# Kernel optimization log

Measured on AMD Instinct MI355X. Metric: run time of the kernel, lower is better.

Reference implementation:

```python
import jax, jax.numpy as jnp
import numpy as np

B, T, D_MODEL = 2, 2048, 2048
N, H, R = 1024, 16, 512
DH = 128          # mem_head_dim (even, fully rotated: rope_dim == DH)
MLAT = 128        # mem_latent_dim
TOPK = 64
EPS = 1e-6
ROPE_BASE = 10000.0


def _rms_norm(x, w):
    var = jnp.mean(jnp.square(x), axis=-1, keepdims=True)
    return x * jax.lax.rsqrt(var + EPS) * w


def _rotate_half(x):
    x1, x2 = jnp.split(x, 2, axis=-1)
    return jnp.concatenate([-x2, x1], axis=-1)


def _apply_rope(x, positions):
    # x: [B, H, L, DH], positions: [L] -> cos/sin [1, 1, L, DH]
    inv_freq = 1.0 / (ROPE_BASE ** (jnp.arange(0, DH, 2, dtype=jnp.float32) / DH))
    freqs = positions.astype(jnp.float32)[:, None] * inv_freq  # [L, DH/2]
    emb = jnp.concatenate([freqs, freqs], axis=-1)             # [L, DH]
    cos = jnp.cos(emb)[None, None].astype(x.dtype)
    sin = jnp.sin(emb)[None, None].astype(x.dtype)
    return x * cos + _rotate_half(x) * sin


def setup_inputs() -> dict:
    key = jax.random.key(0)
    ks = jax.random.split(key, 16)
    s = 0.02
    return {
        "x": jax.random.normal(ks[0], (B, T, D_MODEL), jnp.float32),
        "snapshots": jax.random.normal(ks[1], (B, N, H, R), jnp.float32),
        "snap_positions": jnp.sort(jax.random.randint(ks[2], (N,), 0, T)),
        "token_offset": 0,
        "Wq_down": jax.random.normal(ks[3], (D_MODEL, MLAT), jnp.float32) * s,
        "Wq_up": jax.random.normal(ks[4], (MLAT, H * DH), jnp.float32) * s,
        "Wg_down": jax.random.normal(ks[5], (D_MODEL, MLAT), jnp.float32) * s,
        "Wg_up": jax.random.normal(ks[6], (MLAT, H * DH), jnp.float32) * s,
        "Wo_down": jax.random.normal(ks[7], (H * DH, MLAT), jnp.float32) * s,
        "Wo_up": jax.random.normal(ks[8], (MLAT, D_MODEL), jnp.float32) * s,
        "Wk_up": jax.random.normal(ks[9], (R, DH), jnp.float32) * s,
        "Wv_up": jax.random.normal(ks[10], (R, DH), jnp.float32) * s,
        "q_norm_w": jnp.ones((DH,), jnp.float32),
        "k_norm_w": jnp.ones((DH,), jnp.float32),
        "sink_logit": jnp.zeros((H,), jnp.float32),
    }


def reference(x, snapshots, snap_positions, token_offset,
              Wq_down, Wq_up, Wg_down, Wg_up, Wo_down, Wo_up,
              Wk_up, Wv_up, q_norm_w, k_norm_w, sink_logit):
    b, t, d = x.shape
    _, n, h, r = snapshots.shape
    dh = DH

    # Q path: down/up projection, per-head RMSNorm -> [B, H, T, DH]
    q = ((x @ Wq_down) @ Wq_up).reshape(b, t, h, dh)
    q = _rms_norm(q, q_norm_w).transpose(0, 2, 1, 3)

    # K/V from snapshot latents: [B, N, H, DH] -> [B, H, N, DH]
    k = _rms_norm(snapshots @ Wk_up, k_norm_w).transpose(0, 2, 1, 3)
    v = (snapshots @ Wv_up).transpose(0, 2, 1, 3)

    # dual RoPE: Q by absolute token position, K by snapshot end position
    t_abs = token_offset + jnp.arange(t)
    q = _apply_rope(q, t_abs)
    k = _apply_rope(k, snap_positions)

    scores = jnp.einsum('bhtd,bhnd->bhtn', q, k) / jnp.sqrt(jnp.asarray(dh, q.dtype))

    # causal mask: snapshot strictly before token
    valid = (snap_positions[None, :] < t_abs[:, None])[None, None]  # [1,1,T,N]
    neg_inf = jnp.asarray(-jnp.inf, scores.dtype)
    scores = jnp.where(valid, scores, neg_inf)

    # causal top-k: keep entries >= k-th largest per (b,h,t)
    k_sel = min(TOPK, n)
    if k_sel < n:
        top_vals, _ = jax.lax.top_k(scores, k_sel)
        kth = top_vals[..., -1:]
        scores = jnp.where(scores >= kth, scores, neg_inf)

    # attention sink: extra learned logit per head
    sink = jnp.broadcast_to(sink_logit.astype(jnp.float32)[None, :, None, None], (b, h, t, 1))
    aug = jnp.concatenate([scores.astype(jnp.float32), sink], axis=-1)
    weights = jax.nn.softmax(aug, axis=-1)[..., :n].astype(v.dtype)

    out = jnp.einsum('bhtn,bhnd->bhtd', weights, v)
    out = out.transpose(0, 2, 1, 3).reshape(b, t, h * dh)

    gate = jax.nn.sigmoid((x @ Wg_down) @ Wg_up)
    out = out * gate
    out = (out @ Wo_down) @ Wo_up
    return out
```

## Files before the change

kernel.cpp:

```cpp
#include <hip/hip_runtime.h>

typedef unsigned short u16;
typedef unsigned int u32;
typedef __attribute__((ext_vector_type(8))) short bf16x8;
typedef __attribute__((ext_vector_type(8))) _Float16 f16x8;
typedef __attribute__((ext_vector_type(4))) float f32x4;

__device__ __forceinline__ float b2f(u16 u) {
  union { u32 i; float f; } v; v.i = ((u32)u) << 16; return v.f;
}
__device__ __forceinline__ u16 f2b(float f) {
  u32 u = __builtin_bit_cast(u32, f);
  u32 r = u + 0x7FFFu + ((u >> 16) & 1u);
  return (u16)(r >> 16);
}
__device__ __forceinline__ u16 f2h(float f) {
  return __builtin_bit_cast(u16, (_Float16)f);
}
__device__ __forceinline__ float h2f(u16 u) {
  return (float)__builtin_bit_cast(_Float16, u);
}
__device__ __forceinline__ float wsum(float v) {
  #pragma unroll
  for (int o = 32; o; o >>= 1) v += __shfl_xor(v, o);
  return v;
}
__device__ __forceinline__ float wmax(float v) {
  #pragma unroll
  for (int o = 32; o; o >>= 1) v = fmaxf(v, __shfl_xor(v, o));
  return v;
}

__global__ void k_detect(const u32* x, int* flag) {
  int lane = threadIdx.x;
  u32 w = x[lane * 131 + 7];
  float v = b2f((u16)(w & 0xFFFF));
  float a = fabsf(v);
  bool sane = (a > 1e-3f) && (a < 100.0f);
  unsigned long long m = __ballot(sane);
  if (lane == 0) flag[0] = (__popcll(m) >= 32) ? 0 : 1;
}

struct WtArgs {
  const void* s[8];
  const void* vq; const void* vk; const void* vs;
};
__global__ __launch_bounds__(256)
void k_wtrans_all(WtArgs a, u16* wb, const int* flag) {
  __shared__ u16 Ts[64][66];
  int id = blockIdx.x, t = threadIdx.x, dt = flag[0];
  if (id == 416) {
    u16* dq = wb + 1703936; u16* dk = wb + 1704064; u16* ds = wb + 1704192;
    if (t < 128) dq[t] = dt ? f2b(((const float*)a.vq)[t]) : ((const u16*)a.vq)[t];
    else if (t < 256) dk[t-128] = dt ? f2b(((const float*)a.vk)[t-128]) : ((const u16*)a.vk)[t-128];
    if (t < 16) ds[t] = dt ? f2b(((const float*)a.vs)[t]) : ((const u16*)a.vs)[t];
    return;
  }
  const int cum[9] = {0,64,128,144,160,224,288,352,416};
  const int gsh[8] = {1,1,1,1,5,5,1,5};
  const int Ks[8]  = {2048,2048,512,512,128,128,2048,128};
  const int Ns[8]  = {128,128,128,128,2048,2048,128,2048};
  const unsigned dsts[8] = {0,262144,524288,589824,655360,917504,1179648,1441792};
  int seg = 0;
  #pragma unroll
  for (int i = 0; i < 7; ++i) seg += (id >= cum[i+1]);
  int rel = id - cum[seg];
  int bx = rel & ((1 << gsh[seg]) - 1), by = rel >> gsh[seg];
  int K = Ks[seg], N = Ns[seg];
  const void* src = a.s[seg];
  u16* dst = wb + dsts[seg];
  int col0 = bx * 64, k0 = by * 64;
  int lr = t >> 4, lc = (t & 15) * 4;
  if (dt) {
    #pragma unroll
    for (int p = 0; p < 4; ++p) {
      int kr = lr + p * 16;
      float4 v = *(const float4*)((const float*)src + (size_t)(k0 + kr) * N + col0 + lc);
      Ts[kr][lc+0] = f2b(v.x); Ts[kr][lc+1] = f2b(v.y);
      Ts[kr][lc+2] = f2b(v.z); Ts[kr][lc+3] = f2b(v.w);
    }
  } else {
    #pragma unroll
    for (int p = 0; p < 4; ++p) {
      int kr = lr + p * 16;
      uint2 v = *(const uint2*)((const u16*)src + (size_t)(k0 + kr) * N + col0 + lc);
      *(uint2*)&Ts[kr][lc] = v;
    }
  }
  __syncthreads();
  int col = t >> 2, ks = (t & 3) * 16;
  u16 tmp[16];
  #pragma unroll
  for (int i = 0; i < 16; ++i) tmp[i] = Ts[ks + i][col];
  u16* dp = dst + (size_t)(col0 + col) * K + k0 + ks;
  *(uint4*)dp = *(uint4*)&tmp[0];
  *(uint4*)(dp + 8) = *(uint4*)&tmp[8];
}

template<int JW>
__device__ __forceinline__ void skinny_body(const void* A, const u16* BT, u16* C0, u16* C1,
    int K, bool a32, int m0, int tid, u16 (*As)[40]) {
  int wave = tid >> 6, lane = tid & 63, quad = lane >> 4, l16 = lane & 15;
  f32x4 acc[JW];
  #pragma unroll
  for (int j = 0; j < JW; ++j) acc[j] = (f32x4){0.f,0.f,0.f,0.f};
  int row32 = tid >> 4, kp32 = (tid & 15) * 2;
  int row16 = tid >> 2, kp16 = (tid & 3) * 8;
  float2 pf32 = {};
  uint4 pf16 = {};
  if (a32) pf32 = *(const float2*)((const float*)A + (size_t)(m0+row32)*K + kp32);
  else if (tid < 64) pf16 = *(const uint4*)((const u16*)A + (size_t)(m0+row16)*K + kp16);
  uint4 bf[JW];
  #pragma unroll
  for (int j = 0; j < JW; ++j) {
    int col = wave*(JW*16) + j*16 + l16;
    bf[j] = *(const uint4*)(BT + (size_t)col*K + quad*8);
  }
  for (int k0 = 0; k0 < K; k0 += 32) {
    if (a32) { As[row32][kp32] = f2b(pf32.x); As[row32][kp32+1] = f2b(pf32.y); }
    else if (tid < 64) *(uint4*)&As[row16][kp16] = pf16;
    __syncthreads();
    int k1 = k0 + 32;
    uint4 bn[JW];
    if (k1 < K) {
      if (a32) pf32 = *(const float2*)((const float*)A + (size_t)(m0+row32)*K + k1 + kp32);
      else if (tid < 64) pf16 = *(const uint4*)((const u16*)A + (size_t)(m0+row16)*K + k1 + kp16);
      #pragma unroll
      for (int j = 0; j < JW; ++j) {
        int col = wave*(JW*16) + j*16 + l16;
        bn[j] = *(const uint4*)(BT + (size_t)col*K + k1 + quad*8);
      }
    }
    bf16x8 af = *(const bf16x8*)&As[l16][quad*8];
    #pragma unroll
    for (int j = 0; j < JW; ++j)
      acc[j] = __builtin_amdgcn_mfma_f32_16x16x32_bf16(af, __builtin_bit_cast(bf16x8, bf[j]), acc[j], 0, 0, 0);
    __syncthreads();
    #pragma unroll
    for (int j = 0; j < JW; ++j) bf[j] = bn[j];
  }
  #pragma unroll
  for (int j = 0; j < JW; ++j) {
    int col = wave*(JW*16) + j*16 + l16;
    u16* Cp = (col < 128) ? C0 : C1;
    int cc = col & 127;
    #pragma unroll
    for (int r = 0; r < 4; ++r)
      Cp[(size_t)(m0 + quad*4 + r)*128 + cc] = f2b(acc[j][r]);
  }
}

__device__ __forceinline__ void gemm_up_body(const u16* A, const u16* BT, void* C, int ldc,
    bool o32, int m0, int n0, int tid, u16 (*As)[40]) {
  int wave = tid >> 6, lane = tid & 63, quad = lane >> 4, l16 = lane & 15;
  f32x4 acc[4] = {};
  int row = tid >> 2, kp = (tid & 3) * 8;
  uint4 pa = *(const uint4*)(A + (size_t)(m0+row)*128 + kp);
  uint4 bf[4];
  #pragma unroll
  for (int j = 0; j < 4; ++j)
    bf[j] = *(const uint4*)(BT + (size_t)(n0 + j*16 + l16)*128 + quad*8);
  #pragma unroll
  for (int k0 = 0; k0 < 128; k0 += 32) {
    *(uint4*)&As[row][kp] = pa;
    __syncthreads();
    uint4 bn[4];
    if (k0 < 96) {
      pa = *(const uint4*)(A + (size_t)(m0+row)*128 + k0 + 32 + kp);
      #pragma unroll
      for (int j = 0; j < 4; ++j)
        bn[j] = *(const uint4*)(BT + (size_t)(n0 + j*16 + l16)*128 + k0 + 32 + quad*8);
    }
    bf16x8 af = *(const bf16x8*)&As[wave*16 + l16][quad*8];
    #pragma unroll
    for (int j = 0; j < 4; ++j)
      acc[j] = __builtin_amdgcn_mfma_f32_16x16x32_bf16(af, __builtin_bit_cast(bf16x8, bf[j]), acc[j], 0, 0, 0);
    __syncthreads();
    #pragma unroll
    for (int j = 0; j < 4; ++j) bf[j] = bn[j];
  }
  #pragma unroll
  for (int j = 0; j < 4; ++j) {
    #pragma unroll
    for (int r = 0; r < 4; ++r) {
      size_t ci = (size_t)(m0 + wave*16 + quad*4 + r)*ldc + n0 + j*16 + l16;
      float v = acc[j][r];
      if (o32) ((float*)C)[ci] = v; else ((u16*)C)[ci] = f2b(v);
    }
  }
}

__device__ __forceinline__ void kpost_body(const u16* kraw, u16* kT, const u16* kw,
                                           const int* spos, int rel, int tid) {
  int wave = tid >> 6, lane = tid & 63;
  int rr = rel * 4 + wave;
  int n = (rr >> 4) & 1023, b = rr >> 14, h = rr & 15;
  size_t base = (size_t)rr * 128;
  float x0 = b2f(kraw[base + lane]);
  float x1 = b2f(kraw[base + lane + 64]);
  float ss = wsum(x0*x0 + x1*x1);
  float inv = rsqrtf(ss * (1.0f/128.0f) + 1e-6f);
  float y0 = x0 * inv * b2f(kw[lane]);
  float y1 = x1 * inv * b2f(kw[lane + 64]);
  float pos = (float)spos[n];
  float invf = __expf(-(float)lane * (9.210340371976184f / 64.0f));
  float sn, cs; sincosf(pos * invf, &sn, &cs);
  size_t ob = ((size_t)(b*16 + h) * 1024 + n) * 128;
  kT[ob + lane]      = f2b(y0*cs - y1*sn);
  kT[ob + lane + 64] = f2b(y1*cs + y0*sn);
}

__device__ __forceinline__ void vtrans_body(const u16* vraw, u16* vtt, int bid, int t,
                                            u16 (*Vs)[136]) {
  int ng = bid & 15, bh = bid >> 4;
  int b = bh >> 4, h = bh & 15;
  int n0 = ng * 64;
  int li = t >> 4, seg = (t & 15) * 8;
  #pragma unroll
  for (int p = 0; p < 4; ++p) {
    int i = li + p * 16;
    size_t row = (size_t)(b*1024 + n0 + i) * 16 + h;
    *(uint4*)&Vs[i][seg] = *(const uint4*)(vraw + row*128 + seg);
  }
  __syncthreads();
  int dh = t >> 1, nh = (t & 1) * 32;
  u16 outv[32];
  #pragma unroll
  for (int i = 0; i < 32; ++i) outv[i] = f2h(b2f(Vs[nh + i][dh]));
  u16* dst = vtt + ((size_t)bh * 128 + dh) * 1024 + n0 + nh;
  *(uint4*)(dst)      = *(uint4*)&outv[0];
  *(uint4*)(dst + 8)  = *(uint4*)&outv[8];
  *(uint4*)(dst + 16) = *(uint4*)&outv[16];
  *(uint4*)(dst + 24) = *(uint4*)&outv[24];
}

__global__ __launch_bounds__(256)
void k_down_all(const void* x, const void* snap, const u16* BdT, const u16* BkvT,
                u16* qlat, u16* glat, u16* kraw, u16* vraw, const int* flag) {
  __shared__ u16 As[16][40];
  int id = blockIdx.x;
  bool a32 = flag[0] != 0;
  if (id < 256) skinny_body<4>(x, BdT, qlat, glat, 2048, a32, id*16, threadIdx.x, As);
  else          skinny_body<4>(snap, BkvT, kraw, vraw, 512, a32, (id-256)*16, threadIdx.x, As);
}

__global__ __launch_bounds__(256)
void k_mid_all(const u16* qlat, const u16* glat, const u16* WquT, const u16* WguT,
               u16* qraw, u16* graw, const u16* kraw, u16* kT, const u16* vraw, u16* vtt,
               const u16* ckw, const int* spos, const int* flag) {
  __shared__ u16 smem[64*136];
  int id = blockIdx.x, tid = threadIdx.x;
  if (id < 4096) {
    u16 (*As)[40] = (u16 (*)[40])smem;
    int rel = id & 2047;
    const u16* A  = (id < 2048) ? qlat : glat;
    const u16* BT = (id < 2048) ? WquT : WguT;
    u16* C        = (id < 2048) ? qraw : graw;
    gemm_up_body(A, BT, C, 2048, false, (rel >> 5) * 64, (rel & 31) * 64, tid, As);
  } else if (id < 12288) {
    kpost_body(kraw, kT, ckw, spos, id - 4096, tid);
  } else {
    vtrans_body(vraw, vtt, id - 12288, tid, (u16 (*)[136])smem);
  }
}

__global__ __launch_bounds__(256)
void k_olat(const u16* Ao, const u16* WodT, u16* olat, const int* flag) {
  __shared__ u16 As[16][40];
  skinny_body<2>(Ao, WodT, olat, olat, 2048, false, blockIdx.x*16, threadIdx.x, As);
}

__global__ __launch_bounds__(256)
void k_gemm_up(const u16* A, const u16* BT, void* C, int ldc, const int* flag, int out_dyn) {
  __shared__ u16 As[64][40];
  gemm_up_body(A, BT, C, ldc, out_dyn && flag[0], blockIdx.y*64, blockIdx.x*64, threadIdx.x, As);
}

template<int NJ>
__device__ __forceinline__ void attn_phase2(char* scB, float* rzb, int tl0, int lane,
                                            int nmax, float sinkv, bool do_search) {
  int c0 = lane * 8;
  #pragma unroll 1
  for (int half = 0; half < 2; ++half) {
    float sv[2][NJ]; int key[2][NJ];
    #pragma unroll
    for (int s2 = 0; s2 < 2; ++s2) {
      int tl = tl0 + half*2 + s2;
      int sxor = (tl & 7) << 4;
      const char* rowp = scB + tl*2048;
      uint4 r0 = *(const uint4*)(rowp + ((lane*16) ^ sxor));
      #pragma unroll
      for (int j = 0; j < 8; ++j)
        sv[s2][j] = (c0 + j < nmax) ? h2f(((const u16*)&r0)[j]) : -INFINITY;
      if constexpr (NJ == 16) {
        uint4 r1 = *(const uint4*)(rowp + (1024 + ((lane*16) ^ sxor)));
        #pragma unroll
        for (int j = 0; j < 8; ++j)
          sv[s2][j+8] = (c0 + j + 512 < nmax) ? h2f(((const u16*)&r1)[j]) : -INFINITY;
      }
    }
    float mx[2];
    #pragma unroll
    for (int s2 = 0; s2 < 2; ++s2) {
      float m = -INFINITY;
      #pragma unroll
      for (int j = 0; j < NJ; ++j) {
        float f = sv[s2][j];
        m = fmaxf(m, f);
        float fs = fminf(fmaxf(f * 256.0f + 2048.0f, 0.0f), 4095.0f);
        key[s2][j] = (int)fs;
      }
      mx[s2] = m;
    }
    #pragma unroll
    for (int os = 32; os; os >>= 1) {
      mx[0] = fmaxf(mx[0], __shfl_xor(mx[0], os));
      mx[1] = fmaxf(mx[1], __shfl_xor(mx[1], os));
    }
    int lo2[2] = {0, 0};
    if (do_search) {
      int hi2[2] = {4096, 4096};
      #pragma unroll 1
      for (int it = 0; it < 12; ++it) {
        #pragma unroll
        for (int s2 = 0; s2 < 2; ++s2) {
          int mid = (lo2[s2] + hi2[s2]) >> 1;
          int c = 0;
          #pragma unroll
          for (int j = 0; j < NJ; ++j) c += (int)__popcll(__ballot(key[s2][j] >= mid));
          if (c >= 64) lo2[s2] = mid; else hi2[s2] = mid;
        }
      }
    }
    float m2[2], zp[2];
    u16 wq[2][16];
    #pragma unroll
    for (int s2 = 0; s2 < 2; ++s2) {
      m2[s2] = fmaxf(mx[s2], sinkv);
      float z = 0.f;
      #pragma unroll
      for (int j = 0; j < NJ; ++j) {
        float e = (key[s2][j] >= lo2[s2] && sv[s2][j] > -1e37f) ? __expf(sv[s2][j] - m2[s2]) : 0.f;
        z += e;
        wq[s2][j] = f2h(e);
      }
      zp[s2] = z;
    }
    #pragma unroll
    for (int os = 32; os; os >>= 1) {
      zp[0] += __shfl_xor(zp[0], os);
      zp[1] += __shfl_xor(zp[1], os);
    }
    #pragma unroll
    for (int s2 = 0; s2 < 2; ++s2) {
      int tl = tl0 + half*2 + s2;
      float Z = zp[s2] + __expf(sinkv - m2[s2]);
      if (lane == 0) rzb[tl] = 1.0f / Z;
      int sxor = (tl & 7) << 4;
      char* rowp = scB + tl*2048;
      *(uint4*)(rowp + ((lane*16) ^ sxor)) = *(uint4*)&wq[s2][0];
      if constexpr (NJ == 16)
        *(uint4*)(rowp + (1024 + ((lane*16) ^ sxor))) = *(uint4*)&wq[s2][8];
    }
  }
}

__global__ __launch_bounds__(256, 5)
void k_attn(const u16* qraw, const u16* kT, const u16* vtt, const u16* graw,
            const int* spos, const int* tok, const u16* sink, const u16* qw,
            float* rzg, u16* o) {
  __shared__ u16 sc[16*1024];
  char* scB = (char*)sc;
  u16 (*Qs)[136] = (u16 (*)[136])sc;

  int tid = threadIdx.x;
  int wave = tid >> 6, lane = tid & 63, quad = lane >> 4, l16 = lane & 15;
  int bid0 = blockIdx.x;
  int bid = (bid0 & 7) * 512 + (bid0 >> 3);
  int tile = bid & 127, bh = bid >> 7;
  int h = bh & 15, b = bh >> 4;
  int t0 = tile * 16;
  int tok0 = tok[0];
  float* rzb = rzg + bid * 16;

  {
    float qw0 = b2f(qw[lane]), qw1 = b2f(qw[lane + 64]);
    float invf = __expf(-(float)lane * (9.210340371976184f / 64.0f));
    #pragma unroll 1
    for (int s = 0; s < 4; ++s) {
      int i = wave*4 + s;
      size_t base = ((size_t)(b*2048 + t0 + i))*2048 + h*128;
      float x0 = b2f(qraw[base + lane]);
      float x1 = b2f(qraw[base + lane + 64]);
      float ss = wsum(x0*x0 + x1*x1);
      float inv = rsqrtf(ss * (1.0f/128.0f) + 1e-6f);
      float y0 = x0 * inv * qw0;
      float y1 = x1 * inv * qw1;
      float pos = (float)(tok0 + t0 + i);
      float sn, cs; sincosf(pos * invf, &sn, &cs);
      Qs[i][lane]      = f2b(y0*cs - y1*sn);
      Qs[i][lane + 64] = f2b(y1*cs + y0*sn);
    }
  }
  __syncthreads();

  int nmax;
  {
    int lim = tok0 + t0 + 15;
    int lo = 0, hi = 1024;
    #pragma unroll 1
    while (lo < hi) { int mid = (lo + hi) >> 1; if (spos[mid] < lim) lo = mid + 1; else hi = mid; }
    nmax = lo;
  }
  int pmax = (nmax + 63) >> 6;
  int kkmax = (nmax + 31) >> 5;

  bf16x8 af[4];
  #pragma unroll
  for (int ks = 0; ks < 4; ++ks) af[ks] = *(const bf16x8*)&Qs[l16][ks*32 + quad*8];
  __syncthreads();

  const u16* kTb = kT + (size_t)bh * 131072;
  int nrow = wave*16 + l16;
  uint4 kf[4];
  int pn = 0;
  if (pmax > 0) {
    const u16* kr = kTb + (size_t)nrow * 128 + quad*8;
    #pragma unroll
    for (int ks = 0; ks < 4; ++ks) kf[ks] = *(const uint4*)(kr + ks*32);
    pn = spos[nrow];
  }
  int lim0 = tok0 + t0;
  #pragma unroll 1
  for (int p = 0; p < pmax; ++p) {
    uint4 kn[4];
    int pn_next = 0;
    if (p + 1 < pmax) {
      const u16* kr = kTb + (size_t)((p+1)*64 + nrow) * 128 + quad*8;
      #pragma unroll
      for (int ks = 0; ks < 4; ++ks) kn[ks] = *(const uint4*)(kr + ks*32);
      pn_next = spos[(p+1)*64 + nrow];
    }
    f32x4 c = {};
    __builtin_amdgcn_s_setprio(1);
    #pragma unroll
    for (int ks = 0; ks < 4; ++ks)
      c = __builtin_amdgcn_mfma_f32_16x16x32_bf16(af[ks], __builtin_bit_cast(bf16x8, kf[ks]), c, 0, 0, 0);
    __builtin_amdgcn_s_setprio(0);
    int n = p*64 + nrow;
    #pragma unroll
    for (int r = 0; r < 4; ++r) {
      int t = quad*4 + r;
      float s = c[r] * 0.08838834764831845f;
      if (pn >= lim0 + t) s = -INFINITY;
      *(u16*)(scB + ((t*2048 + n*2) ^ ((t&7)<<4))) = f2h(s);
    }
    #pragma unroll
    for (int ks = 0; ks < 4; ++ks) kf[ks] = kn[ks];
    pn = pn_next;
  }
  __syncthreads();

  float sinkv = b2f(sink[h]);

  int tl0 = wave*4;
  bool do_search = (nmax > 64);
  if (nmax > 512) attn_phase2<16>(scB, rzb, tl0, lane, nmax, sinkv, do_search);
  else            attn_phase2<8> (scB, rzb, tl0, lane, nmax, sinkv, do_search);
  __syncthreads();

  int dh0 = wave * 32;
  float rz4[4];
  u16 g0r[4], g1r[4];
  #pragma unroll
  for (int r = 0; r < 4; ++r) {
    int t = quad*4 + r;
    rz4[r] = rzb[t];
    size_t oi = ((size_t)(b*2048 + t0 + t))*2048 + h*128 + dh0 + l16;
    g0r[r] = graw[oi];
    g1r[r] = graw[oi + 16];
  }

  const u16* vbase = vtt + (size_t)bh * 131072;
  const u16* vr0 = vbase + (size_t)(dh0 + l16)*1024 + quad*8;
  const u16* vr1 = vbase + (size_t)(dh0 + 16 + l16)*1024 + quad*8;
  f32x4 acc0 = {}, acc1 = {};
  uint4 vf0 = *(const uint4*)vr0;
  uint4 vf1 = *(const uint4*)vr1;
  int axor = (l16&7) << 4;
  const char* arow = scB + l16*2048;
  #pragma unroll 1
  for (int kk = 0; kk < kkmax; ++kk) {
    uint4 vn0, vn1;
    if (kk + 1 < kkmax) {
      vn0 = *(const uint4*)(vr0 + (kk+1)*32);
      vn1 = *(const uint4*)(vr1 + (kk+1)*32);
    }
    f16x8 a = *(const f16x8*)(arow + ((kk*64 + quad*16) ^ axor));
    __builtin_amdgcn_s_setprio(1);
    acc0 = __builtin_amdgcn_mfma_f32_16x16x32_f16(a, __builtin_bit_cast(f16x8, vf0), acc0, 0, 0, 0);
    acc1 = __builtin_amdgcn_mfma_f32_16x16x32_f16(a, __builtin_bit_cast(f16x8, vf1), acc1, 0, 0, 0);
    __builtin_amdgcn_s_setprio(0);
    vf0 = vn0; vf1 = vn1;
  }

  #pragma unroll
  for (int r = 0; r < 4; ++r) {
    int t = quad*4 + r;
    size_t oi = ((size_t)(b*2048 + t0 + t))*2048 + h*128 + dh0 + l16;
    float g0 = 1.0f / (1.0f + __expf(-b2f(g0r[r])));
    float g1 = 1.0f / (1.0f + __expf(-b2f(g1r[r])));
    o[oi] = f2b(acc0[r] * rz4[r] * g0);
    o[oi + 16] = f2b(acc1[r] * rz4[r] * g1);
  }
}

extern "C" void kernel_launch(void* const* d_in, const int* in_sizes, int n_in,
                              void* d_out, int out_size, void* d_ws, size_t ws_size,
                              hipStream_t stream) {
  char* ws = (char*)d_ws;
  int* flag = (int*)(ws + 0);
  u16* wb = (u16*)(ws + 4096);

  u16* BdT  = wb + 0;
  u16* BkvT = wb + 524288;
  u16* WquT = wb + 655360;
  u16* WguT = wb + 917504;
  u16* WodT = wb + 1179648;
  u16* WouT = wb + 1441792;
  u16* cqw  = wb + 1703936;
  u16* ckw  = wb + 1704064;
  u16* csink= wb + 1704192;

  const size_t O_QLAT = 4198400;
  const size_t O_GLAT = 5246976;
  const size_t O_QRAW = 6295552;
  const size_t O_GRAW = 23072768;
  const size_t O_KRAW = 39849984;
  const size_t O_VRAW = 48238592;
  const size_t O_KT   = 56627200;
  const size_t O_VTT  = 65015808;

  const int* spos = (const int*)d_in[2];
  const int* tok  = (const int*)d_in[3];

  k_detect<<<1, 64, 0, stream>>>((const u32*)d_in[0], flag);

  WtArgs wa;
  wa.s[0] = d_in[4];  wa.s[1] = d_in[6];  wa.s[2] = d_in[10]; wa.s[3] = d_in[11];
  wa.s[4] = d_in[5];  wa.s[5] = d_in[7];  wa.s[6] = d_in[8];  wa.s[7] = d_in[9];
  wa.vq = d_in[12]; wa.vk = d_in[13]; wa.vs = d_in[14];
  k_wtrans_all<<<417, 256, 0, stream>>>(wa, wb, flag);

  k_down_all<<<2304, 256, 0, stream>>>(d_in[0], d_in[1], BdT, BkvT,
      (u16*)(ws + O_QLAT), (u16*)(ws + O_GLAT), (u16*)(ws + O_KRAW), (u16*)(ws + O_VRAW), flag);

  k_mid_all<<<12800, 256, 0, stream>>>((const u16*)(ws + O_QLAT), (const u16*)(ws + O_GLAT),
      WquT, WguT, (u16*)(ws + O_QRAW), (u16*)(ws + O_GRAW),
      (const u16*)(ws + O_KRAW), (u16*)(ws + O_KT), (const u16*)(ws + O_VRAW), (u16*)(ws + O_VTT),
      ckw, spos, flag);

  k_attn<<<4096, 256, 0, stream>>>((const u16*)(ws + O_QRAW), (const u16*)(ws + O_KT),
      (const u16*)(ws + O_VTT), (const u16*)(ws + O_GRAW), spos, tok, csink, cqw,
      (float*)(ws + O_GLAT), (u16*)(ws + O_GRAW));

  k_olat<<<256, 256, 0, stream>>>((const u16*)(ws + O_GRAW), WodT, (u16*)(ws + O_QLAT), flag);
  k_gemm_up<<<dim3(32,64), 256, 0, stream>>>((const u16*)(ws + O_QLAT), WouT, d_out, 2048, flag, 1);
}
```

Baseline: 507.2 us.

## Precompute RoPE tables and per-tile nmax, batch four rows in top-k softmax

Result: slower. 588.8 us (+16.1%).

```diff
diff --git a/kernel.cpp b/kernel.cpp
--- a/kernel.cpp
+++ b/kernel.cpp
@@ -23,11 +23,6 @@
 __device__ __forceinline__ float wsum(float v) {
   #pragma unroll
   for (int o = 32; o; o >>= 1) v += __shfl_xor(v, o);
-  return v;
-}
-__device__ __forceinline__ float wmax(float v) {
-  #pragma unroll
-  for (int o = 32; o; o >>= 1) v = fmaxf(v, __shfl_xor(v, o));
   return v;
 }
 
@@ -39,6 +34,34 @@
   bool sane = (a > 1e-3f) && (a < 100.0f);
   unsigned long long m = __ballot(sane);
   if (lane == 0) flag[0] = (__popcll(m) >= 32) ? 0 : 1;
+}
+
+__global__ __launch_bounds__(256)
+void k_tab(const int* spos, const int* tok, float2* qtab, float2* ktab, int* nmaxg) {
+  if (blockIdx.x == 768) {
+    int t = threadIdx.x;
+    if (t < 128) {
+      int lim = tok[0] + t * 16 + 15;
+      int lo = 0, hi = 1024;
+      #pragma unroll 1
+      while (lo < hi) { int mid = (lo + hi) >> 1; if (spos[mid] < lim) lo = mid + 1; else hi = mid; }
+      nmaxg[t] = lo;
+    }
+    return;
+  }
+  int id = blockIdx.x * 4 + (threadIdx.x >> 6);
+  int lane = threadIdx.x & 63;
+  float invf = __expf(-(float)lane * (9.210340371976184f / 64.0f));
+  if (id < 2048) {
+    float pos = (float)(tok[0] + id);
+    float sn, cs; sincosf(pos * invf, &sn, &cs);
+    qtab[id * 64 + lane] = make_float2(cs, sn);
+  } else {
+    int n = id - 2048;
+    float pos = (float)spos[n];
+    float sn, cs; sincosf(pos * invf, &sn, &cs);
+    ktab[n * 64 + lane] = make_float2(cs, sn);
+  }
 }
 
 struct WtArgs {
@@ -191,7 +214,7 @@
 }
 
 __device__ __forceinline__ void kpost_body(const u16* kraw, u16* kT, const u16* kw,
-                                           const int* spos, int rel, int tid) {
+                                           const float2* ktab, int rel, int tid) {
   int wave = tid >> 6, lane = tid & 63;
   int rr = rel * 4 + wave;
   int n = (rr >> 4) & 1023, b = rr >> 14, h = rr & 15;
@@ -202,12 +225,10 @@
   float inv = rsqrtf(ss * (1.0f/128.0f) + 1e-6f);
   float y0 = x0 * inv * b2f(kw[lane]);
   float y1 = x1 * inv * b2f(kw[lane + 64]);
-  float pos = (float)spos[n];
-  float invf = __expf(-(float)lane * (9.210340371976184f / 64.0f));
-  float sn, cs; sincosf(pos * invf, &sn, &cs);
+  float2 cs2 = ktab[n * 64 + lane];
   size_t ob = ((size_t)(b*16 + h) * 1024 + n) * 128;
-  kT[ob + lane]      = f2b(y0*cs - y1*sn);
-  kT[ob + lane + 64] = f2b(y1*cs + y0*sn);
+  kT[ob + lane]      = f2b(y0*cs2.x - y1*cs2.y);
+  kT[ob + lane + 64] = f2b(y1*cs2.x + y0*cs2.y);
 }
 
 __device__ __forceinline__ void vtrans_body(const u16* vraw, u16* vtt, int bid, int t,
@@ -247,7 +268,7 @@
 __global__ __launch_bounds__(256)
 void k_mid_all(const u16* qlat, const u16* glat, const u16* WquT, const u16* WguT,
                u16* qraw, u16* graw, const u16* kraw, u16* kT, const u16* vraw, u16* vtt,
-               const u16* ckw, const int* spos, const int* flag) {
+               const u16* ckw, const float2* ktab, const int* flag) {
   __shared__ u16 smem[64*136];
   int id = blockIdx.x, tid = threadIdx.x;
   if (id < 4096) {
@@ -258,7 +279,7 @@
     u16* C        = (id < 2048) ? qraw : graw;
     gemm_up_body(A, BT, C, 2048, false, (rel >> 5) * 64, (rel & 31) * 64, tid, As);
   } else if (id < 12288) {
-    kpost_body(kraw, kT, ckw, spos, id - 4096, tid);
+    kpost_body(kraw, kT, ckw, ktab, id - 4096, tid);
   } else {
     vtrans_body(vraw, vtt, id - 12288, tid, (u16 (*)[136])smem);
   }
@@ -278,97 +299,91 @@
 
 template<int NJ>
 __device__ __forceinline__ void attn_phase2(char* scB, float* rzb, int tl0, int lane,
-                                            int nmax, float sinkv, bool do_search) {
-  int c0 = lane * 8;
-  #pragma unroll 1
-  for (int half = 0; half < 2; ++half) {
-    float sv[2][NJ]; int key[2][NJ];
-    #pragma unroll
-    for (int s2 = 0; s2 < 2; ++s2) {
-      int tl = tl0 + half*2 + s2;
-      int sxor = (tl & 7) << 4;
-      const char* rowp = scB + tl*2048;
-      uint4 r0 = *(const uint4*)(rowp + ((lane*16) ^ sxor));
+                                            float sinkv, bool do_search) {
+  float sv[4][NJ]; int key[4][NJ];
+  #pragma unroll
+  for (int s = 0; s < 4; ++s) {
+    int tl = tl0 + s;
+    int sxor = (tl & 7) << 4;
+    const char* rowp = scB + tl*2048;
+    uint4 r0 = *(const uint4*)(rowp + ((lane*16) ^ sxor));
+    #pragma unroll
+    for (int j = 0; j < 8; ++j) sv[s][j] = h2f(((const u16*)&r0)[j]);
+    if constexpr (NJ == 16) {
+      uint4 r1 = *(const uint4*)(rowp + (1024 + ((lane*16) ^ sxor)));
       #pragma unroll
-      for (int j = 0; j < 8; ++j)
-        sv[s2][j] = (c0 + j < nmax) ? h2f(((const u16*)&r0)[j]) : -INFINITY;
-      if constexpr (NJ == 16) {
-        uint4 r1 = *(const uint4*)(rowp + (1024 + ((lane*16) ^ sxor)));
+      for (int j = 0; j < 8; ++j) sv[s][j+8] = h2f(((const u16*)&r1)[j]);
+    }
+  }
+  float mx[4];
+  #pragma unroll
+  for (int s = 0; s < 4; ++s) {
+    float m = -INFINITY;
+    #pragma unroll
+    for (int j = 0; j < NJ; ++j) {
+      float f = sv[s][j];
+      m = fmaxf(m, f);
+      float fs = fminf(fmaxf(f * 256.0f + 2048.0f, 0.0f), 4095.0f);
+      key[s][j] = (int)fs;
+    }
+    mx[s] = m;
+  }
+  #pragma unroll
+  for (int os = 32; os; os >>= 1) {
+    #pragma unroll
+    for (int s = 0; s < 4; ++s) mx[s] = fmaxf(mx[s], __shfl_xor(mx[s], os));
+  }
+  int lo4[4] = {0,0,0,0};
+  if (do_search) {
+    int hi4[4] = {4096,4096,4096,4096};
+    #pragma unroll 1
+    for (int it = 0; it < 12; ++it) {
+      #pragma unroll
+      for (int s = 0; s < 4; ++s) {
+        int mid = (lo4[s] + hi4[s]) >> 1;
+        int c = 0;
         #pragma unroll
-        for (int j = 0; j < 8; ++j)
-          sv[s2][j+8] = (c0 + j + 512 < nmax) ? h2f(((const u16*)&r1)[j]) : -INFINITY;
+        for (int j = 0; j < NJ; ++j) c += (int)__popcll(__ballot(key[s][j] >= mid));
+        if (c >= 64) lo4[s] = mid; else hi4[s] = mid;
       }
     }
-    float mx[2];
-    #pragma unroll
-    for (int s2 = 0; s2 < 2; ++s2) {
-      float m = -INFINITY;
-      #pragma unroll
-      for (int j = 0; j < NJ; ++j) {
-        float f = sv[s2][j];
-        m = fmaxf(m, f);
-        float fs = fminf(fmaxf(f * 256.0f + 2048.0f, 0.0f), 4095.0f);
-        key[s2][j] = (int)fs;
-      }
-      mx[s2] = m;
-    }
-    #pragma unroll
-    for (int os = 32; os; os >>= 1) {
-      mx[0] = fmaxf(mx[0], __shfl_xor(mx[0], os));
-      mx[1] = fmaxf(mx[1], __shfl_xor(mx[1], os));
-    }
-    int lo2[2] = {0, 0};
-    if (do_search) {
-      int hi2[2] = {4096, 4096};
-      #pragma unroll 1
-      for (int it = 0; it < 12; ++it) {
-        #pragma unroll
-        for (int s2 = 0; s2 < 2; ++s2) {
-          int mid = (lo2[s2] + hi2[s2]) >> 1;
-          int c = 0;
-          #pragma unroll
-          for (int j = 0; j < NJ; ++j) c += (int)__popcll(__ballot(key[s2][j] >= mid));
-          if (c >= 64) lo2[s2] = mid; else hi2[s2] = mid;
-        }
-      }
-    }
-    float m2[2], zp[2];
-    u16 wq[2][16];
-    #pragma unroll
-    for (int s2 = 0; s2 < 2; ++s2) {
-      m2[s2] = fmaxf(mx[s2], sinkv);
-      float z = 0.f;
-      #pragma unroll
-      for (int j = 0; j < NJ; ++j) {
-        float e = (key[s2][j] >= lo2[s2] && sv[s2][j] > -1e37f) ? __expf(sv[s2][j] - m2[s2]) : 0.f;
-        z += e;
-        wq[s2][j] = f2h(e);
-      }
-      zp[s2] = z;
-    }
-    #pragma unroll
-    for (int os = 32; os; os >>= 1) {
-      zp[0] += __shfl_xor(zp[0], os);
-      zp[1] += __shfl_xor(zp[1], os);
-    }
-    #pragma unroll
-    for (int s2 = 0; s2 < 2; ++s2) {
-      int tl = tl0 + half*2 + s2;
-      float Z = zp[s2] + __expf(sinkv - m2[s2]);
-      if (lane == 0) rzb[tl] = 1.0f / Z;
-      int sxor = (tl & 7) << 4;
-      char* rowp = scB + tl*2048;
-      *(uint4*)(rowp + ((lane*16) ^ sxor)) = *(uint4*)&wq[s2][0];
-      if constexpr (NJ == 16)
-        *(uint4*)(rowp + (1024 + ((lane*16) ^ sxor))) = *(uint4*)&wq[s2][8];
-    }
+  }
+  float m2[4], zp[4];
+  u16 wq[4][16];
+  #pragma unroll
+  for (int s = 0; s < 4; ++s) {
+    m2[s] = fmaxf(mx[s], sinkv);
+    float z = 0.f;
+    #pragma unroll
+    for (int j = 0; j < NJ; ++j) {
+      float e = (key[s][j] >= lo4[s] && sv[s][j] > -1e37f) ? __expf(sv[s][j] - m2[s]) : 0.f;
+      z += e;
+      wq[s][j] = f2h(e);
+    }
+    zp[s] = z;
+  }
+  #pragma unroll
+  for (int os = 32; os; os >>= 1) {
+    #pragma unroll
+    for (int s = 0; s < 4; ++s) zp[s] += __shfl_xor(zp[s], os);
+  }
+  #pragma unroll
+  for (int s = 0; s < 4; ++s) {
+    int tl = tl0 + s;
+    float Z = zp[s] + __expf(sinkv - m2[s]);
+    if (lane == 0) rzb[tl] = 1.0f / Z;
+    int sxor = (tl & 7) << 4;
+    char* rowp = scB + tl*2048;
+    *(uint4*)(rowp + ((lane*16) ^ sxor)) = *(uint4*)&wq[s][0];
+    if constexpr (NJ == 16)
+      *(uint4*)(rowp + (1024 + ((lane*16) ^ sxor))) = *(uint4*)&wq[s][8];
   }
 }
 
 __global__ __launch_bounds__(256, 5)
 void k_attn(const u16* qraw, const u16* kT, const u16* vtt, const u16* graw,
             const int* spos, const int* tok, const u16* sink, const u16* qw,
-            float* rzg, u16* o) {
+            const float2* qtab, const int* nmaxg, float* rzg, u16* o) {
   __shared__ u16 sc[16*1024];
   char* scB = (char*)sc;
   u16 (*Qs)[136] = (u16 (*)[136])sc;
@@ -377,7 +392,8 @@
   int wave = tid >> 6, lane = tid & 63, quad = lane >> 4, l16 = lane & 15;
   int bid0 = blockIdx.x;
   int bid = (bid0 & 7) * 512 + (bid0 >> 3);
-  int tile = bid & 127, bh = bid >> 7;
+  int tile = (bid & 127) ^ 127;
+  int bh = bid >> 7;
   int h = bh & 15, b = bh >> 4;
   int t0 = tile * 16;
   int tok0 = tok[0];
@@ -385,7 +401,6 @@
 
   {
     float qw0 = b2f(qw[lane]), qw1 = b2f(qw[lane + 64]);
-    float invf = __expf(-(float)lane * (9.210340371976184f / 64.0f));
     #pragma unroll 1
     for (int s = 0; s < 4; ++s) {
       int i = wave*4 + s;
@@ -396,24 +411,17 @@
       float inv = rsqrtf(ss * (1.0f/128.0f) + 1e-6f);
       float y0 = x0 * inv * qw0;
       float y1 = x1 * inv * qw1;
-      float pos = (float)(tok0 + t0 + i);
-      float sn, cs; sincosf(pos * invf, &sn, &cs);
-      Qs[i][lane]      = f2b(y0*cs - y1*sn);
-      Qs[i][lane + 64] = f2b(y1*cs + y0*sn);
+      float2 cs2 = qtab[(size_t)(t0 + i)*64 + lane];
+      Qs[i][lane]      = f2b(y0*cs2.x - y1*cs2.y);
+      Qs[i][lane + 64] = f2b(y1*cs2.x + y0*cs2.y);
     }
   }
   __syncthreads();
 
-  int nmax;
-  {
-    int lim = tok0 + t0 + 15;
-    int lo = 0, hi = 1024;
-    #pragma unroll 1
-    while (lo < hi) { int mid = (lo + hi) >> 1; if (spos[mid] < lim) lo = mid + 1; else hi = mid; }
-    nmax = lo;
-  }
+  int nmax = nmaxg[tile];
   int pmax = (nmax + 63) >> 6;
   int kkmax = (nmax + 31) >> 5;
+  int ncols = (nmax > 512) ? 1024 : 512;
 
   bf16x8 af[4];
   #pragma unroll
@@ -459,14 +467,27 @@
     for (int ks = 0; ks < 4; ++ks) kf[ks] = kn[ks];
     pn = pn_next;
   }
+  {
+    int c0f = pmax * 64;
+    int nchunk = (ncols - c0f) >> 3;
+    if (nchunk > 0) {
+      int row = tid >> 4, trc = tid & 15;
+      uint4 ninf; ninf.x = ninf.y = ninf.z = ninf.w = 0xFC00FC00u;
+      char* rp = scB + row*2048;
+      int sx = (row & 7) << 4;
+      #pragma unroll 1
+      for (int c8 = trc; c8 < nchunk; c8 += 16)
+        *(uint4*)(rp + (((c0f + c8*8)*2) ^ sx)) = ninf;
+    }
+  }
   __syncthreads();
 
   float sinkv = b2f(sink[h]);
 
   int tl0 = wave*4;
   bool do_search = (nmax > 64);
-  if (nmax > 512) attn_phase2<16>(scB, rzb, tl0, lane, nmax, sinkv, do_search);
-  else            attn_phase2<8> (scB, rzb, tl0, lane, nmax, sinkv, do_search);
+  if (ncols == 1024) attn_phase2<16>(scB, rzb, tl0, lane, sinkv, do_search);
+  else               attn_phase2<8> (scB, rzb, tl0, lane, sinkv, do_search);
   __syncthreads();
 
   int dh0 = wave * 32;
@@ -540,11 +561,17 @@
   const size_t O_VRAW = 48238592;
   const size_t O_KT   = 56627200;
   const size_t O_VTT  = 65015808;
+  const size_t O_QTAB = 73404416;
+  const size_t O_KTAB = 74452992;
+  const size_t O_NMAX = 74977280;
 
   const int* spos = (const int*)d_in[2];
   const int* tok  = (const int*)d_in[3];
 
   k_detect<<<1, 64, 0, stream>>>((const u32*)d_in[0], flag);
+
+  k_tab<<<769, 256, 0, stream>>>(spos, tok, (float2*)(ws + O_QTAB), (float2*)(ws + O_KTAB),
+      (int*)(ws + O_NMAX));
 
   WtArgs wa;
   wa.s[0] = d_in[4];  wa.s[1] = d_in[6];  wa.s[2] = d_in[10]; wa.s[3] = d_in[11];
@@ -558,10 +585,11 @@
   k_mid_all<<<12800, 256, 0, stream>>>((const u16*)(ws + O_QLAT), (const u16*)(ws + O_GLAT),
       WquT, WguT, (u16*)(ws + O_QRAW), (u16*)(ws + O_GRAW),
       (const u16*)(ws + O_KRAW), (u16*)(ws + O_KT), (const u16*)(ws + O_VRAW), (u16*)(ws + O_VTT),
-      ckw, spos, flag);
+      ckw, (const float2*)(ws + O_KTAB), flag);
 
   k_attn<<<4096, 256, 0, stream>>>((const u16*)(ws + O_QRAW), (const u16*)(ws + O_KT),
       (const u16*)(ws + O_VTT), (const u16*)(ws + O_GRAW), spos, tok, csink, cqw,
+      (const float2*)(ws + O_QTAB), (const int*)(ws + O_NMAX),
       (float*)(ws + O_GLAT), (u16*)(ws + O_GRAW));
 
   k_olat<<<256, 256, 0, stream>>>((const u16*)(ws + O_GRAW), WodT, (u16*)(ws + O_QLAT), flag);
```
